# Kernel optimization log

Hardware: AMD Instinct MI355X
Metric: run time of the kernel (lower is better)

Reference implementation:

```python
import jax, jax.numpy as jnp
import numpy as np
from jax import lax

D_MODEL = 512
D_INNER = 1024   # expand=2
D_STATE = 16
D_CONV = 4
DT_RANK = 32     # ceil(d_model/16)
D_FFN = 2048
EPS = 1e-6


def _layernorm(x, g, b):
    mu = jnp.mean(x, axis=-1, keepdims=True)
    var = jnp.mean((x - mu) ** 2, axis=-1, keepdims=True)
    return (x - mu) * lax.rsqrt(var + EPS) * g + b


def _mamba(x, in_w, conv_w, conv_b, xproj_w, dt_w, dt_b, A_log, D_vec, out_w):
    # x: [B, L, d_model]
    B, L, _ = x.shape
    xz = jnp.einsum('bld,ed->ble', x, in_w)           # [B, L, 2*d_inner]
    xc, z = xz[..., :D_INNER], xz[..., D_INNER:]
    # causal depthwise conv over time
    xt = xc.transpose(0, 2, 1)                        # [B, d_inner, L]
    kern = conv_w[:, None, :]                         # [d_inner, 1, d_conv]
    xt = lax.conv_general_dilated(xt, kern, (1,), [(D_CONV - 1, 0)],
                                  feature_group_count=D_INNER)
    xc = jax.nn.silu(xt.transpose(0, 2, 1) + conv_b)  # [B, L, d_inner]
    # input-dependent SSM parameters
    x_dbl = jnp.einsum('bld,ed->ble', xc, xproj_w)    # [B, L, dt_rank+2*d_state]
    dt = x_dbl[..., :DT_RANK]
    Bm = x_dbl[..., DT_RANK:DT_RANK + D_STATE]
    Cm = x_dbl[..., DT_RANK + D_STATE:]
    delta = jax.nn.softplus(jnp.einsum('blr,dr->bld', dt, dt_w) + dt_b)  # [B, L, d_inner]
    A = -jnp.exp(A_log)                               # [d_inner, d_state]

    def step(h, inp):
        d_t, u_t, b_t, c_t = inp                      # [B,di],[B,di],[B,ds],[B,ds]
        dA = jnp.exp(d_t[:, :, None] * A)             # [B, di, ds]
        dBu = (d_t * u_t)[:, :, None] * b_t[:, None, :]
        h = dA * h + dBu
        y = jnp.einsum('bds,bs->bd', h, c_t)
        return h, y

    h0 = jnp.zeros((B, D_INNER, D_STATE), x.dtype)
    xs = (delta.transpose(1, 0, 2), xc.transpose(1, 0, 2),
          Bm.transpose(1, 0, 2), Cm.transpose(1, 0, 2))
    _, ys = lax.scan(step, h0, xs)                    # [L, B, d_inner]
    y = ys.transpose(1, 0, 2) + xc * D_vec
    y = y * jax.nn.silu(z)
    return jnp.einsum('ble,de->bld', y, out_w)        # [B, L, d_model]


def setup_inputs() -> dict:
    key = jax.random.key(0)
    ks = iter(jax.random.split(key, 40))
    B, S, T = 8, 512, 1024

    def nrm(shape, scale=0.02):
        return jax.random.normal(next(ks), shape, dtype=jnp.float32) * scale

    def mamba_params(prefix):
        A_log = jnp.log(jnp.broadcast_to(jnp.arange(1, D_STATE + 1, dtype=jnp.float32),
                                         (D_INNER, D_STATE)))
        return {
            prefix + '_in_w': nrm((2 * D_INNER, D_MODEL)),
            prefix + '_conv_w': nrm((D_INNER, D_CONV), 0.1),
            prefix + '_conv_b': jnp.zeros((D_INNER,), jnp.float32),
            prefix + '_xproj_w': nrm((DT_RANK + 2 * D_STATE, D_INNER)),
            prefix + '_dt_w': nrm((D_INNER, DT_RANK), 0.1),
            prefix + '_dt_b': jnp.full((D_INNER,), -4.0, jnp.float32),
            prefix + '_A_log': A_log,
            prefix + '_D_vec': jnp.ones((D_INNER,), jnp.float32),
            prefix + '_out_w': nrm((D_MODEL, D_INNER)),
        }

    inp = {
        'tgt': jax.random.normal(next(ks), (B, S, D_MODEL), dtype=jnp.float32),
        'memory': jax.random.normal(next(ks), (B, T, D_MODEL), dtype=jnp.float32),
    }
    inp.update(mamba_params('self'))
    inp.update(mamba_params('cross'))
    inp.update({
        'ln1_g': jnp.ones((D_MODEL,), jnp.float32), 'ln1_b': jnp.zeros((D_MODEL,), jnp.float32),
        'ln2_g': jnp.ones((D_MODEL,), jnp.float32), 'ln2_b': jnp.zeros((D_MODEL,), jnp.float32),
        'ln3_g': jnp.ones((D_MODEL,), jnp.float32), 'ln3_b': jnp.zeros((D_MODEL,), jnp.float32),
        'ffn_w1': nrm((D_FFN, D_MODEL)), 'ffn_b1': jnp.zeros((D_FFN,), jnp.float32),
        'ffn_w2': nrm((D_MODEL, D_FFN)), 'ffn_b2': jnp.zeros((D_MODEL,), jnp.float32),
    })
    return inp


def reference(tgt, memory,
              self_in_w, self_conv_w, self_conv_b, self_xproj_w, self_dt_w, self_dt_b,
              self_A_log, self_D_vec, self_out_w,
              cross_in_w, cross_conv_w, cross_conv_b, cross_xproj_w, cross_dt_w, cross_dt_b,
              cross_A_log, cross_D_vec, cross_out_w,
              ln1_g, ln1_b, ln2_g, ln2_b, ln3_g, ln3_b,
              ffn_w1, ffn_b1, ffn_w2, ffn_b2):
    S = tgt.shape[1]
    # self-Mamba block (post-norm, dropout=0)
    t2 = _mamba(tgt, self_in_w, self_conv_w, self_conv_b, self_xproj_w,
                self_dt_w, self_dt_b, self_A_log, self_D_vec, self_out_w)
    t = _layernorm(tgt + t2, ln1_g, ln1_b)
    # cross-Mamba: scan over [memory; tgt], keep last S steps
    cat = jnp.concatenate([memory, t], axis=1)
    c2 = _mamba(cat, cross_in_w, cross_conv_w, cross_conv_b, cross_xproj_w,
                cross_dt_w, cross_dt_b, cross_A_log, cross_D_vec, cross_out_w)[:, -S:]
    t = _layernorm(t + c2, ln2_g, ln2_b)
    # positionwise FFN
    f = jnp.einsum('bld,fd->blf', t, ffn_w1) + ffn_b1
    f = jax.nn.relu(f)
    f = jnp.einsum('blf,df->bld', f, ffn_w2) + ffn_b2
    t = _layernorm(t + f, ln3_g, ln3_b)
    return t
```

## Files before the change

kernel.cpp:

```cpp
#include <hip/hip_runtime.h>
#include <math.h>

#define DM    512
#define DI    1024
#define DSN   16
#define DTR   32
#define DFFN  2048
#define BB    8
#define SS    512
#define TTM   1024
#define LCAT  1536
#define CONV_R 8

#define ACT_NONE     0
#define ACT_RELU     1
#define ACT_DELTA    3
#define ACT_XDBL     4

typedef __attribute__((ext_vector_type(8))) short short8;
typedef __attribute__((ext_vector_type(8))) unsigned short ushort8;
typedef __attribute__((ext_vector_type(4))) float f32x4;

#define L2E 1.4426950408889634f

__device__ __forceinline__ unsigned short f2b(float f) {
    unsigned int u = __float_as_uint(f);
    return (unsigned short)((u + 0x7FFFu + ((u >> 16) & 1u)) >> 16);
}
__device__ __forceinline__ float b2f(unsigned short h) {
    return __uint_as_float(((unsigned int)h) << 16);
}
__device__ __forceinline__ float fast_softplus(float v) {
    return (v > 20.f) ? v : __logf(1.f + __expf(v));
}
__device__ __forceinline__ float fexp2(float x) {
#if __has_builtin(__builtin_amdgcn_exp2f)
    return __builtin_amdgcn_exp2f(x);
#else
    float r; asm("v_exp_f32 %0, %1" : "=v"(r) : "v"(x)); return r;
#endif
}
__device__ __forceinline__ float frcp(float x) {
    return __builtin_amdgcn_rcpf(x);
}
__device__ __forceinline__ void gld16(const void* g, void* l) {
    __builtin_amdgcn_global_load_lds(
        (const __attribute__((address_space(1))) void*)g,
        (__attribute__((address_space(3))) void*)l, 16, 0, 0);
}

__device__ __forceinline__ int map_row(int m, int mb, int bs, int ro) {
    int q = m / mb;
    return q * bs + ro + (m - q * mb);
}

__global__ __launch_bounds__(256) void mgemm_kernel(
    const unsigned short* __restrict__ A, int mb, int bs, int ro,
    const unsigned short* __restrict__ W, const float* __restrict__ bias,
    float* __restrict__ Cf, unsigned short* __restrict__ Cb,
    float* __restrict__ C2, float* __restrict__ Cf2,
    int N, int K, int act,
    int omb, int obs, int oro, int ldc, int nofs, int pstr,
    int ysplit, int amb2, int abs2, int aro2, int wofs2,
    int omb2, int obs2, int oro2, int nofs2)
{
    __shared__ __align__(16) unsigned short As[128 * 64];
    __shared__ __align__(16) unsigned short Bs[128 * 64];
    int tid = threadIdx.x;
    int lane = tid & 63, wave = tid >> 6;
    int wy = wave >> 1, wx = wave & 1;
    int bx = blockIdx.x, by = blockIdx.y;
    int nx = gridDim.x, ny = gridDim.y;
    const unsigned short* Wp = W;
    if (ysplit) {
        if (by >= ysplit) {
            by -= ysplit; ny = gridDim.y - ysplit;
            mb = amb2; bs = abs2; ro = aro2; Wp += wofs2;
            omb = omb2; obs = obs2; oro = oro2; nofs = nofs2;
        } else ny = ysplit;
    }
    int f = by * nx + bx;
    int xcd = f & 7, j2 = f >> 3;
    int bandh = ny >> 3;
    int m0 = (xcd * bandh + j2 / nx) * 128;
    int n0 = (j2 % nx) * 128;
    int Kh = K / gridDim.z;
    int kbeg = blockIdx.z * Kh, kend = kbeg + Kh;
    float* Cfo = Cf;
    const float* biaso = bias;
    if (blockIdx.z) { Cfo = Cf2 + (size_t)(blockIdx.z - 1) * pstr; biaso = nullptr; }

    unsigned aoff[4], boff[4];
    unsigned short* la[4];
    unsigned short* lb[4];
    #pragma unroll
    for (int j = 0; j < 4; j++) {
        int c  = wave * 256 + j * 64 + lane;
        int r  = c >> 3;
        int q  = c & 7;
        int g  = q ^ (r & 7);
        int arow = map_row(m0 + r, mb, bs, ro);
        aoff[j] = (unsigned)(arow * K + g * 8);
        boff[j] = (unsigned)((n0 + r) * K + g * 8);
        la[j] = As + (size_t)(wave * 256 + j * 64) * 8;
        lb[j] = Bs + (size_t)(wave * 256 + j * 64) * 8;
    }
    int fm = lane & 15, fg = lane >> 4;
    int sw = fg ^ (fm & 3);
    int b2 = (fm >> 2) & 1;
    const unsigned short* arp = As + ((size_t)(wy * 64 + fm) * 8 + sw) * 8;
    const unsigned short* brp = Bs + ((size_t)(wx * 64 + fm) * 8 + sw) * 8;

    f32x4 acc[4][4];
    #pragma unroll
    for (int i = 0; i < 4; i++)
        #pragma unroll
        for (int j = 0; j < 4; j++) acc[i][j] = 0.f;

    for (int k0 = kbeg; k0 < kend; k0 += 64) {
        #pragma unroll
        for (int j = 0; j < 4; j++) {
            gld16(A  + aoff[j] + k0, la[j]);
            gld16(Wp + boff[j] + k0, lb[j]);
        }
        __syncthreads();
        #pragma unroll
        for (int h = 0; h < 2; h++) {
            int ho = ((h ^ b2) * 32);
            short8 af[4], bfr[4];
            #pragma unroll
            for (int t = 0; t < 4; t++) af[t]  = *(const short8*)(arp + ho + t * 1024);
            #pragma unroll
            for (int t = 0; t < 4; t++) bfr[t] = *(const short8*)(brp + ho + t * 1024);
            #pragma unroll
            for (int i = 0; i < 4; i++)
                #pragma unroll
                for (int j = 0; j < 4; j++)
                    acc[i][j] = __builtin_amdgcn_mfma_f32_16x16x32_bf16(af[i], bfr[j], acc[i][j], 0, 0, 0);
        }
        __syncthreads();
    }

    int en = lane & 15, em = (lane >> 4) * 4;
    if (act == ACT_XDBL) {
        size_t zb = (size_t)blockIdx.z * omb;
        #pragma unroll
        for (int j = 0; j < 4; j++) {
            int n = n0 + wx * 64 + j * 16 + en;
            if (n >= 64) continue;
            #pragma unroll
            for (int i = 0; i < 4; i++) {
                int mbase = m0 + wy * 64 + i * 16 + em;
                #pragma unroll
                for (int r = 0; r < 4; r++)
                    C2[(zb + mbase + r) * 64 + n] = acc[i][j][r];
            }
        }
        return;
    }
    if (act == ACT_DELTA) {
        #pragma unroll
        for (int j = 0; j < 4; j++) {
            int n = n0 + wx * 64 + j * 16 + en;
            float bv = bias[n];
            #pragma unroll
            for (int i = 0; i < 4; i++) {
                int mbase = m0 + wy * 64 + i * 16 + em;
                #pragma unroll
                for (int r = 0; r < 4; r++) {
                    float v = acc[i][j][r] + bv;
                    Cb[(size_t)(mbase + r) * 1024 + n] = f2b(fast_softplus(v));
                }
            }
        }
        return;
    }
    #pragma unroll
    for (int j = 0; j < 4; j++) {
        int n = n0 + wx * 64 + j * 16 + en;
        float bv = biaso ? biaso[n] : 0.f;
        #pragma unroll
        for (int i = 0; i < 4; i++) {
            int mbase = m0 + wy * 64 + i * 16 + em;
            #pragma unroll
            for (int r = 0; r < 4; r++) {
                float v = acc[i][j][r] + bv;
                if (act == ACT_RELU) v = v > 0.f ? v : 0.f;
                int orow = map_row(mbase + r, omb, obs, oro);
                size_t off = (size_t)orow * ldc + nofs + n;
                if (Cb) Cb[off] = f2b(v);
                else    Cfo[off] = v;
            }
        }
    }
}

__global__ __launch_bounds__(256) void xdbl_combine(
    const float* __restrict__ pxd, unsigned short* __restrict__ dtb,
    float* __restrict__ bcout, int M, int Z)
{
    int idx = blockIdx.x * 256 + threadIdx.x;
    int m = idx >> 4, n4 = idx & 15;
    int n = n4 * 4;
    float4 s = make_float4(0.f, 0.f, 0.f, 0.f);
    for (int z = 0; z < Z; z++) {
        float4 p = *(const float4*)(pxd + ((size_t)z * M + m) * 64 + n);
        s.x += p.x; s.y += p.y; s.z += p.z; s.w += p.w;
    }
    if (n < 32) {
        ((ushort4*)(dtb + (size_t)m * 64))[n4] =
            make_ushort4(f2b(s.x), f2b(s.y), f2b(s.z), f2b(s.w));
    } else {
        *(float4*)(bcout + (size_t)m * 32 + (n - 32)) = s;
        ((ushort4*)(dtb + (size_t)m * 64))[n4] = make_ushort4(0, 0, 0, 0);
    }
}

struct PrepPtrs {
    const float* tgt; const float* mem;
    const float* w[6];
    const float* xpj_s; const float* xpj_c;
    const float* dtw_s; const float* dtw_c;
    unsigned short* tgtb; unsigned short* catb; unsigned short* wb;
    unsigned short* xprojb_s; unsigned short* xprojb_c;
    unsigned short* dtwb_s; unsigned short* dtwb_c;
};
__global__ __launch_bounds__(256) void prep_kernel(PrepPtrs p)
{
    int u = blockIdx.x * 256 + threadIdx.x;
    if (u < 524288) {
        float4 v = ((const float4*)p.tgt)[u];
        ((ushort4*)p.tgtb)[u] = make_ushort4(f2b(v.x), f2b(v.y), f2b(v.z), f2b(v.w));
        return;
    }
    if (u < 1572864) {
        int f = u - 524288;
        int b = f >> 17, rem = f & 131071;
        float4 v = ((const float4*)p.mem)[f];
        ((ushort4*)p.catb)[(size_t)b * 196608 + rem] =
            make_ushort4(f2b(v.x), f2b(v.y), f2b(v.z), f2b(v.w));
        return;
    }
    if (u < 2883584) {
        const int cum[7] = {0, 262144, 524288, 655360, 786432, 1048576, 1310720};
        int i = u - 1572864;
        int seg = 0;
        #pragma unroll
        for (int s = 1; s < 6; s++) seg += (i >= cum[s]);
        float4 v = ((const float4*)p.w[seg])[i - cum[seg]];
        ((ushort4*)p.wb)[i] = make_ushort4(f2b(v.x), f2b(v.y), f2b(v.z), f2b(v.w));
        return;
    }
    if (u < 2949120) {
        int i = u - 2883584;
        const float* src = p.xpj_s;
        unsigned short* dst = p.xprojb_s;
        if (i >= 32768) { i -= 32768; src = p.xpj_c; dst = p.xprojb_c; }
        int n = i >> 8;
        ushort4 o = make_ushort4(0, 0, 0, 0);
        if (n < 64) {
            float4 v = ((const float4*)src)[i];
            o = make_ushort4(f2b(v.x), f2b(v.y), f2b(v.z), f2b(v.w));
        }
        ((ushort4*)dst)[i] = o;
        return;
    }
    {
        int i = u - 2949120;
        const float* src = p.dtw_s;
        unsigned short* dst = p.dtwb_s;
        if (i >= 16384) { i -= 16384; src = p.dtw_c; dst = p.dtwb_c; }
        int n = i >> 4, c = (i & 15) * 4;
        ushort4 o = make_ushort4(0, 0, 0, 0);
        if (c < 32) {
            float4 v = *(const float4*)(src + n * 32 + c);
            o = make_ushort4(f2b(v.x), f2b(v.y), f2b(v.z), f2b(v.w));
        }
        ((ushort4*)dst)[i] = o;
    }
}

__global__ __launch_bounds__(256) void conv_silu_kernel(
    const unsigned short* __restrict__ xz,
    const float* __restrict__ cw,
    const float* __restrict__ cb,
    unsigned short* __restrict__ xc, int L, int total)
{
    int idx = blockIdx.x * blockDim.x + threadIdx.x;
    if (idx >= total) return;
    int d8 = idx & 127;
    int d0 = d8 * 8;
    int t  = idx >> 7;
    int nq = L / CONV_R;
    int b  = t / nq;
    int l0 = (t - b * nq) * CONV_R;
    size_t rbase = (size_t)b * L + l0;

    float4 wv[8];
    #pragma unroll
    for (int j = 0; j < 8; j++) wv[j] = *(const float4*)(cw + (d0 + j) * 4);
    float bias[8];
    {
        float4 c0 = ((const float4*)(cb + d0))[0];
        float4 c1 = ((const float4*)(cb + d0))[1];
        bias[0]=c0.x; bias[1]=c0.y; bias[2]=c0.z; bias[3]=c0.w;
        bias[4]=c1.x; bias[5]=c1.y; bias[6]=c1.z; bias[7]=c1.w;
    }
    ushort8 win[CONV_R + 3];
    #pragma unroll
    for (int k = 0; k < 3; k++) {
        ushort8 z;
        #pragma unroll
        for (int j = 0; j < 8; j++) z[j] = 0;
        win[k] = (l0 - 3 + k >= 0)
            ? *(const ushort8*)(xz + (rbase - 3 + k) * 2048 + d0) : z;
    }
    #pragma unroll
    for (int i = 0; i < CONV_R; i++)
        win[3 + i] = *(const ushort8*)(xz + (rbase + i) * 2048 + d0);

    const float* w = (const float*)&wv[0];
    #pragma unroll
    for (int i = 0; i < CONV_R; i++) {
        float acc[8];
        #pragma unroll
        for (int j = 0; j < 8; j++) acc[j] = bias[j];
        #pragma unroll
        for (int k = 0; k < 4; k++) {
            ushort8 v = win[i + k];
            #pragma unroll
            for (int j = 0; j < 8; j++)
                acc[j] = fmaf(b2f(v[j]), w[j * 4 + k], acc[j]);
        }
        ushort8 o;
        #pragma unroll
        for (int j = 0; j < 8; j++)
            o[j] = f2b(acc[j] * frcp(1.f + __expf(-acc[j])));
        *(ushort8*)(xc + (rbase + i) * 1024 + d0) = o;
    }
}

__global__ __launch_bounds__(256) void scan_part1(
    const unsigned short* __restrict__ delta, const unsigned short* __restrict__ xc,
    const float* __restrict__ bc, const float* __restrict__ A_log,
    float* __restrict__ part_h, float* __restrict__ part_s, int L, int CH, int NCr)
{
    int tid = threadIdx.x;
    int dblk = blockIdx.x & 3;
    int rest = blockIdx.x >> 2;
    int c    = rest % NCr;
    int b    = rest / NCr;
    if (c == NCr - 1) return;
    int d    = dblk * 256 + tid;
    float A2[DSN];
    {
        const float4* ap = (const float4*)(A_log + d * DSN);
        #pragma unroll
        for (int q = 0; q < 4; q++) {
            float4 a4 = ap[q];
            A2[q*4+0] = -__expf(a4.x) * L2E;
            A2[q*4+1] = -__expf(a4.y) * L2E;
            A2[q*4+2] = -__expf(a4.z) * L2E;
            A2[q*4+3] = -__expf(a4.w) * L2E;
        }
    }
    float h[DSN];
    #pragma unroll
    for (int s = 0; s < DSN; s++) h[s] = 0.f;
    float ssum = 0.f;
    int l0 = c * CH;
    for (int l = l0; l < l0 + CH; l++) {
        size_t r = (size_t)b * L + l;
        float4 bq[4];
        const float4* bp = (const float4*)(bc + r * 32);
        #pragma unroll
        for (int q = 0; q < 4; q++) bq[q] = bp[q];
        const float* Bm = (const float*)&bq[0];
        float dl = b2f(delta[r * DI + d]);
        float u  = b2f(xc[r * DI + d]);
        float du = dl * u;
        ssum += dl;
        #pragma unroll
        for (int s = 0; s < DSN; s++)
            h[s] = fmaf(fexp2(dl * A2[s]), h[s], du * Bm[s]);
    }
    size_t base = ((size_t)(b * NCr + c) * DI + d) * DSN;
    #pragma unroll
    for (int q = 0; q < 4; q++)
        ((float4*)(part_h + base))[q] = make_float4(h[q*4], h[q*4+1], h[q*4+2], h[q*4+3]);
    part_s[(size_t)(b * NCr + c) * DI + d] = ssum;
}

__global__ __launch_bounds__(256) void scan_combine(
    const float* __restrict__ A_log,
    float* __restrict__ part_h, const float* __restrict__ part_s, int NCr)
{
    int idx = blockIdx.x * 256 + threadIdx.x;
    int s  = idx & (DSN - 1);
    int dd = (idx >> 4) & (DI - 1);
    int b  = idx >> 14;
    float A2 = -__expf(A_log[dd * DSN + s]) * L2E;
    float h = 0.f;
    size_t sbase = (size_t)b * NCr * DI + dd;
    size_t hbase = ((size_t)b * NCr * DI + dd) * DSN + s;
    for (int c = 0; c < NCr; c++) {
        float ph = part_h[hbase];
        float S  = part_s[sbase];
        part_h[hbase] = h;
        h = fmaf(fexp2(A2 * S), h, ph);
        hbase += (size_t)DI * DSN;
        sbase += DI;
    }
}

__global__ __launch_bounds__(256) void scan_part2(
    const unsigned short* __restrict__ delta, const unsigned short* __restrict__ xc,
    const float* __restrict__ bc, const unsigned short* __restrict__ xz,
    const float* __restrict__ A_log, const float* __restrict__ Dv,
    const float* __restrict__ part_h,
    unsigned short* __restrict__ out, int L, int CH, int NCr, int c0, int lmin)
{
    int tid = threadIdx.x;
    int dblk = blockIdx.x & 3;
    int rest = blockIdx.x >> 2;
    int ncp  = NCr - c0;
    int c    = c0 + rest % ncp;
    int b    = rest / ncp;
    int d    = dblk * 256 + tid;
    float A2[DSN];
    {
        const float4* ap = (const float4*)(A_log + d * DSN);
        #pragma unroll
        for (int q = 0; q < 4; q++) {
            float4 a4 = ap[q];
            A2[q*4+0] = -__expf(a4.x) * L2E;
            A2[q*4+1] = -__expf(a4.y) * L2E;
            A2[q*4+2] = -__expf(a4.z) * L2E;
            A2[q*4+3] = -__expf(a4.w) * L2E;
        }
    }
    float Dvd = Dv[d];
    size_t base = ((size_t)(b * NCr + c) * DI + d) * DSN;
    float h4[4][4];
    #pragma unroll
    for (int q = 0; q < 4; q++) *((float4*)h4[q]) = ((const float4*)(part_h + base))[q];
    float h[DSN];
    #pragma unroll
    for (int s = 0; s < DSN; s++) h[s] = h4[s >> 2][s & 3];
    int l0 = c * CH;
    for (int l = l0; l < l0 + CH; l++) {
        size_t r = (size_t)b * L + l;
        float4 bq[8];
        const float4* bp = (const float4*)(bc + r * 32);
        #pragma unroll
        for (int q = 0; q < 8; q++) bq[q] = bp[q];
        const float* Bm = (const float*)&bq[0];
        const float* Cm = Bm + DSN;
        float dl = b2f(delta[r * DI + d]);
        float u  = b2f(xc[r * DI + d]);
        float du = dl * u;
        float y = 0.f;
        #pragma unroll
        for (int s = 0; s < DSN; s++) {
            h[s] = fmaf(fexp2(dl * A2[s]), h[s], du * Bm[s]);
            y = fmaf(h[s], Cm[s], y);
        }
        if (l >= lmin) {
            float z = b2f(xz[r * 2048 + DI + d]);
            float sil = z * frcp(1.f + __expf(-z));
            out[r * DI + d] = f2b((y + u * Dvd) * sil);
        }
    }
}

__global__ __launch_bounds__(128) void addln_kernel(
    const float* __restrict__ a, int amb, int absd, int aro, int lda,
    const float* __restrict__ bsrc, const float* __restrict__ parts, int nparts, int pstr,
    const float* __restrict__ g, const float* __restrict__ be,
    float* __restrict__ outf, int omb, int obsd, int oro, int ldo,
    unsigned short* __restrict__ outb, int bmb, int bbsd, int bro, int ldb)
{
    int m = blockIdx.x, t = threadIdx.x;
    int ar = map_row(m, amb, absd, aro);
    float4 x4 = ((const float4*)(a + (size_t)ar * lda))[t];
    float4 y4 = ((const float4*)(bsrc + (size_t)m * DM))[t];
    float v[4] = {x4.x + y4.x, x4.y + y4.y, x4.z + y4.z, x4.w + y4.w};
    for (int p = 0; p < nparts; p++) {
        float4 z4 = ((const float4*)(parts + (size_t)p * pstr + (size_t)m * DM))[t];
        v[0] += z4.x; v[1] += z4.y; v[2] += z4.z; v[3] += z4.w;
    }
    float sum = v[0] + v[1] + v[2] + v[3];
    float sq  = v[0]*v[0] + v[1]*v[1] + v[2]*v[2] + v[3]*v[3];
    #pragma unroll
    for (int o = 32; o > 0; o >>= 1) {
        sum += __shfl_down(sum, o);
        sq  += __shfl_down(sq, o);
    }
    __shared__ float s0[2], s1[2];
    if ((t & 63) == 0) { s0[t >> 6] = sum; s1[t >> 6] = sq; }
    __syncthreads();
    float tot = s0[0] + s0[1];
    float tsq = s1[0] + s1[1];
    float mu = tot * (1.f / DM);
    float var = tsq * (1.f / DM) - mu * mu;
    float rs = rsqrtf(var + 1e-6f);
    float4 g4 = ((const float4*)g)[t];
    float4 b4 = ((const float4*)be)[t];
    float o0 = (v[0] - mu) * rs * g4.x + b4.x;
    float o1 = (v[1] - mu) * rs * g4.y + b4.y;
    float o2 = (v[2] - mu) * rs * g4.z + b4.z;
    float o3 = (v[3] - mu) * rs * g4.w + b4.w;
    if (outf) {
        int orow = map_row(m, omb, obsd, oro);
        ((float4*)(outf + (size_t)orow * ldo))[t] = make_float4(o0, o1, o2, o3);
    }
    if (outb) {
        int brow = map_row(m, bmb, bbsd, bro);
        ((ushort4*)(outb + (size_t)brow * ldb))[t] =
            make_ushort4(f2b(o0), f2b(o1), f2b(o2), f2b(o3));
    }
}

static void run_scan(const unsigned short* dltb, const unsigned short* xcb, const float* bc,
                     const unsigned short* xzb, const float* A_log, const float* Dv,
                     float* part_h, float* part_s, unsigned short* out, int L, int NCr,
                     int c0, int lmin, hipStream_t stream)
{
    int CH = L / NCr;
    int blocks1 = BB * NCr * (DI / 256);
    scan_part1<<<blocks1, 256, 0, stream>>>(dltb, xcb, bc, A_log, part_h, part_s, L, CH, NCr);
    scan_combine<<<BB * DI * DSN / 256, 256, 0, stream>>>(A_log, part_h, part_s, NCr);
    int blocks2 = BB * (NCr - c0) * (DI / 256);
    scan_part2<<<blocks2, 256, 0, stream>>>(dltb, xcb, bc, xzb, A_log, Dv, part_h, out, L, CH, NCr, c0, lmin);
}

extern "C" void kernel_launch(void* const* d_in, const int* in_sizes, int n_in,
                              void* d_out, int out_size, void* d_ws, size_t ws_size,
                              hipStream_t stream)
{
    const float* tgt       = (const float*)d_in[0];
    const float* memory    = (const float*)d_in[1];
    const float* s_in_w    = (const float*)d_in[2];
    const float* s_conv_w  = (const float*)d_in[3];
    const float* s_conv_b  = (const float*)d_in[4];
    const float* s_xproj_w = (const float*)d_in[5];
    const float* s_dt_w    = (const float*)d_in[6];
    const float* s_dt_b    = (const float*)d_in[7];
    const float* s_A_log   = (const float*)d_in[8];
    const float* s_D_vec   = (const float*)d_in[9];
    const float* s_out_w   = (const float*)d_in[10];
    const float* c_in_w    = (const float*)d_in[11];
    const float* c_conv_w  = (const float*)d_in[12];
    const float* c_conv_b  = (const float*)d_in[13];
    const float* c_xproj_w = (const float*)d_in[14];
    const float* c_dt_w    = (const float*)d_in[15];
    const float* c_dt_b    = (const float*)d_in[16];
    const float* c_A_log   = (const float*)d_in[17];
    const float* c_D_vec   = (const float*)d_in[18];
    const float* c_out_w   = (const float*)d_in[19];
    const float* ln1_g     = (const float*)d_in[20];
    const float* ln1_b     = (const float*)d_in[21];
    const float* ln2_g     = (const float*)d_in[22];
    const float* ln2_b     = (const float*)d_in[23];
    const float* ln3_g     = (const float*)d_in[24];
    const float* ln3_b     = (const float*)d_in[25];
    const float* ffn_w1    = (const float*)d_in[26];
    const float* ffn_b1    = (const float*)d_in[27];
    const float* ffn_w2    = (const float*)d_in[28];
    const float* ffn_b2    = (const float*)d_in[29];
    float* outp = (float*)d_out;

    float* ws     = (float*)d_ws;
    float* bc     = ws;
    float* t1     = bc     + 393216;
    float* tbuf   = t1     + 2097152;
    float* part_h = tbuf   + 2097152;
    float* proj   = part_h;
    float* pparts = part_h + 2097152;
    float* pxd    = part_h;
    float* part_s = part_h + 8388608;
    unsigned short* ub      = (unsigned short*)(part_s + 524288);
    unsigned short* dltb    = ub;
    unsigned short* catb    = dltb    + 12582912;
    unsigned short* tgtb    = catb    + 6291456;
    unsigned short* xzb     = tgtb    + 2097152;
    unsigned short* xcb     = xzb     + 25165824;
    unsigned short* ygb     = xcb     + 12582912;
    unsigned short* tbbf    = ygb     + 12582912;
    unsigned short* s_in_wb = tbbf    + 2097152;
    unsigned short* c_in_wb = s_in_wb + 1048576;
    unsigned short* s_out_wb= c_in_wb + 1048576;
    unsigned short* c_out_wb= s_out_wb+ 524288;
    unsigned short* w1b     = c_out_wb+ 524288;
    unsigned short* w2b     = w1b     + 1048576;
    unsigned short* xprojb_s= w2b     + 1048576;
    unsigned short* xprojb_c= xprojb_s+ 131072;
    unsigned short* dtwb_s  = xprojb_c+ 131072;
    unsigned short* dtwb_c  = dtwb_s  + 65536;
    unsigned short* dtb     = dtwb_c  + 65536;
    unsigned short* fbuf    = xzb;
    float* ffnout  = (float*)dltb;
    float* fparts  = ffnout + 2097152;

    {
        PrepPtrs pp;
        pp.tgt = tgt; pp.mem = memory;
        pp.w[0]=s_in_w; pp.w[1]=c_in_w; pp.w[2]=s_out_w; pp.w[3]=c_out_w; pp.w[4]=ffn_w1; pp.w[5]=ffn_w2;
        pp.xpj_s = s_xproj_w; pp.xpj_c = c_xproj_w;
        pp.dtw_s = s_dt_w;    pp.dtw_c = c_dt_w;
        pp.tgtb = tgtb; pp.catb = catb; pp.wb = s_in_wb;
        pp.xprojb_s = xprojb_s; pp.xprojb_c = xprojb_c;
        pp.dtwb_s = dtwb_s; pp.dtwb_c = dtwb_c;
        prep_kernel<<<11648, 256, 0, stream>>>(pp);
    }

    mgemm_kernel<<<dim3(2048/128, 4096/128), 256, 0, stream>>>(
        tgtb, 4096, 0, 0, s_in_wb, nullptr, nullptr, xzb, nullptr, nullptr, 2048, 512, ACT_NONE,
        4096, 0, 0, 2048, 0, 0,  0, 0,0,0, 0, 0,0,0, 0);
    conv_silu_kernel<<<(BB*(SS/CONV_R)*128 + 255)/256, 256, 0, stream>>>(
        xzb, s_conv_w, s_conv_b, xcb, SS, BB*(SS/CONV_R)*128);
    mgemm_kernel<<<dim3(1, 4096/128, 4), 256, 0, stream>>>(
        xcb, 4096, 0, 0, xprojb_s, nullptr, nullptr, nullptr, pxd, nullptr, 128, 1024, ACT_XDBL,
        4096, 0, 0, 0, 0, 0,  0, 0,0,0, 0, 0,0,0, 0);
    xdbl_combine<<<4096*16/256, 256, 0, stream>>>(pxd, dtb, bc, 4096, 4);
    mgemm_kernel<<<dim3(1024/128, 4096/128), 256, 0, stream>>>(
        dtb, 4096, 0, 0, dtwb_s, s_dt_b, nullptr, dltb, nullptr, nullptr, 1024, 64, ACT_DELTA,
        4096, 0, 0, 1024, 0, 0,  0, 0,0,0, 0, 0,0,0, 0);
    run_scan(dltb, xcb, bc, xzb, s_A_log, s_D_vec, part_h, part_s, ygb, SS, 32, 0, 0, stream);
    mgemm_kernel<<<dim3(512/128, 4096/128, 4), 256, 0, stream>>>(
        ygb, 4096, 0, 0, s_out_wb, nullptr, proj, nullptr, nullptr, pparts, 512, 1024, ACT_NONE,
        4096, 0, 0, 512, 0, 2097152,  0, 0,0,0, 0, 0,0,0, 0);
    addln_kernel<<<4096, 128, 0, stream>>>(
        tgt, 4096, 0, 0, DM, proj, pparts, 3, 2097152, ln1_g, ln1_b,
        t1, 4096, 0, 0, DM, catb, 512, 1536, 1024, DM);

    mgemm_kernel<<<dim3(1024/128, 96 + 32), 256, 0, stream>>>(
        catb, 12288, 0, 0, c_in_wb, nullptr, nullptr, xzb, nullptr, nullptr, 2048, 512, ACT_NONE,
        12288, 0, 0, 2048, 0, 0,
        96, 512, 1536, 1024, 1024 * 512, 512, 1536, 1024, 1024);
    conv_silu_kernel<<<(BB*(LCAT/CONV_R)*128 + 255)/256, 256, 0, stream>>>(
        xzb, c_conv_w, c_conv_b, xcb, LCAT, BB*(LCAT/CONV_R)*128);
    mgemm_kernel<<<dim3(1, 12288/128, 4), 256, 0, stream>>>(
        xcb, 12288, 0, 0, xprojb_c, nullptr, nullptr, nullptr, pxd, nullptr, 128, 1024, ACT_XDBL,
        12288, 0, 0, 0, 0, 0,  0, 0,0,0, 0, 0,0,0, 0);
    xdbl_combine<<<12288*16/256, 256, 0, stream>>>(pxd, dtb, bc, 12288, 4);
    mgemm_kernel<<<dim3(1024/128, 12288/128), 256, 0, stream>>>(
        dtb, 12288, 0, 0, dtwb_c, c_dt_b, nullptr, dltb, nullptr, nullptr, 1024, 64, ACT_DELTA,
        12288, 0, 0, 1024, 0, 0,  0, 0,0,0, 0, 0,0,0, 0);
    run_scan(dltb, xcb, bc, xzb, c_A_log, c_D_vec, part_h, part_s, ygb, LCAT, 32, 21, 1024, stream);
    mgemm_kernel<<<dim3(512/128, 4096/128, 4), 256, 0, stream>>>(
        ygb, 512, 1536, 1024, c_out_wb, nullptr, proj, nullptr, nullptr, pparts, 512, 1024, ACT_NONE,
        4096, 0, 0, 512, 0, 2097152,  0, 0,0,0, 0, 0,0,0, 0);
    addln_kernel<<<4096, 128, 0, stream>>>(
        t1, 4096, 0, 0, DM, proj, pparts, 3, 2097152, ln2_g, ln2_b,
        tbuf, 4096, 0, 0, DM, tbbf, 4096, 0, 0, DM);

    mgemm_kernel<<<dim3(2048/128, 4096/128), 256, 0, stream>>>(
        tbbf, 4096, 0, 0, w1b, ffn_b1, nullptr, fbuf, nullptr, nullptr, 2048, 512, ACT_RELU,
        4096, 0, 0, 2048, 0, 0,  0, 0,0,0, 0, 0,0,0, 0);
    mgemm_kernel<<<dim3(512/128, 4096/128, 4), 256, 0, stream>>>(
        fbuf, 4096, 0, 0, w2b, ffn_b2, ffnout, nullptr, nullptr, fparts, 512, 2048, ACT_NONE,
        4096, 0, 0, 512, 0, 2097152,  0, 0,0,0, 0, 0,0,0, 0);
    addln_kernel<<<4096, 128, 0, stream>>>(
        tbuf, 4096, 0, 0, DM, ffnout, fparts, 3, 2097152, ln3_g, ln3_b,
        outp, 4096, 0, 0, DM, nullptr, 0, 0, 0, 0);
}
```

Measured before the change: 498.9 us.

## Stage scan B/C in shared memory, prefetch inputs, and double chunk count

```diff
diff --git a/kernel.cpp b/kernel.cpp
--- a/kernel.cpp
+++ b/kernel.cpp
@@ -345,12 +345,19 @@
     const float* __restrict__ bc, const float* __restrict__ A_log,
     float* __restrict__ part_h, float* __restrict__ part_s, int L, int CH, int NCr)
 {
+    __shared__ float bcs[24 * 16];
     int tid = threadIdx.x;
     int dblk = blockIdx.x & 3;
     int rest = blockIdx.x >> 2;
     int c    = rest % NCr;
     int b    = rest / NCr;
     if (c == NCr - 1) return;
+    int l0 = c * CH;
+    for (int i = tid; i < CH * 16; i += 256) {
+        int lr = i >> 4, s = i & 15;
+        bcs[i] = bc[((size_t)b * L + l0 + lr) * 32 + s];
+    }
+    __syncthreads();
     int d    = dblk * 256 + tid;
     float A2[DSN];
     {
@@ -368,21 +375,22 @@
     #pragma unroll
     for (int s = 0; s < DSN; s++) h[s] = 0.f;
     float ssum = 0.f;
-    int l0 = c * CH;
-    for (int l = l0; l < l0 + CH; l++) {
-        size_t r = (size_t)b * L + l;
-        float4 bq[4];
-        const float4* bp = (const float4*)(bc + r * 32);
-        #pragma unroll
-        for (int q = 0; q < 4; q++) bq[q] = bp[q];
-        const float* Bm = (const float*)&bq[0];
-        float dl = b2f(delta[r * DI + d]);
-        float u  = b2f(xc[r * DI + d]);
-        float du = dl * u;
-        ssum += dl;
+    size_t rb = (size_t)b * L + l0;
+    float dl = b2f(delta[rb * DI + d]);
+    float u  = b2f(xc[rb * DI + d]);
+    for (int i = 0; i < CH; i++) {
+        float cdl = dl, cu = u;
+        if (i + 1 < CH) {
+            size_t rn = rb + i + 1;
+            dl = b2f(delta[rn * DI + d]);
+            u  = b2f(xc[rn * DI + d]);
+        }
+        const float* Bm = bcs + i * 16;
+        float du = cdl * cu;
+        ssum += cdl;
         #pragma unroll
         for (int s = 0; s < DSN; s++)
-            h[s] = fmaf(fexp2(dl * A2[s]), h[s], du * Bm[s]);
+            h[s] = fmaf(fexp2(cdl * A2[s]), h[s], du * Bm[s]);
     }
     size_t base = ((size_t)(b * NCr + c) * DI + d) * DSN;
     #pragma unroll
@@ -420,12 +428,17 @@
     const float* __restrict__ part_h,
     unsigned short* __restrict__ out, int L, int CH, int NCr, int c0, int lmin)
 {
+    __shared__ float bcs[24 * 32];
     int tid = threadIdx.x;
     int dblk = blockIdx.x & 3;
     int rest = blockIdx.x >> 2;
     int ncp  = NCr - c0;
     int c    = c0 + rest % ncp;
     int b    = rest / ncp;
+    int l0 = c * CH;
+    for (int i = tid; i < CH * 32; i += 256)
+        bcs[i] = bc[((size_t)b * L + l0) * 32 + i];
+    __syncthreads();
     int d    = dblk * 256 + tid;
     float A2[DSN];
     {
@@ -447,28 +460,30 @@
     float h[DSN];
     #pragma unroll
     for (int s = 0; s < DSN; s++) h[s] = h4[s >> 2][s & 3];
-    int l0 = c * CH;
-    for (int l = l0; l < l0 + CH; l++) {
-        size_t r = (size_t)b * L + l;
-        float4 bq[8];
-        const float4* bp = (const float4*)(bc + r * 32);
-        #pragma unroll
-        for (int q = 0; q < 8; q++) bq[q] = bp[q];
-        const float* Bm = (const float*)&bq[0];
+    size_t rb = (size_t)b * L + l0;
+    float dl = b2f(delta[rb * DI + d]);
+    float u  = b2f(xc[rb * DI + d]);
+    float z  = b2f(xz[rb * 2048 + DI + d]);
+    for (int i = 0; i < CH; i++) {
+        float cdl = dl, cu = u, cz = z;
+        if (i + 1 < CH) {
+            size_t rn = rb + i + 1;
+            dl = b2f(delta[rn * DI + d]);
+            u  = b2f(xc[rn * DI + d]);
+            z  = b2f(xz[rn * 2048 + DI + d]);
+        }
+        const float* Bm = bcs + i * 32;
         const float* Cm = Bm + DSN;
-        float dl = b2f(delta[r * DI + d]);
-        float u  = b2f(xc[r * DI + d]);
-        float du = dl * u;
+        float du = cdl * cu;
         float y = 0.f;
         #pragma unroll
         for (int s = 0; s < DSN; s++) {
-            h[s] = fmaf(fexp2(dl * A2[s]), h[s], du * Bm[s]);
+            h[s] = fmaf(fexp2(cdl * A2[s]), h[s], du * Bm[s]);
             y = fmaf(h[s], Cm[s], y);
         }
-        if (l >= lmin) {
-            float z = b2f(xz[r * 2048 + DI + d]);
-            float sil = z * frcp(1.f + __expf(-z));
-            out[r * DI + d] = f2b((y + u * Dvd) * sil);
+        if (l0 + i >= lmin) {
+            float sil = cz * frcp(1.f + __expf(-cz));
+            out[(rb + i) * DI + d] = f2b((y + cu * Dvd) * sil);
         }
     }
 }
@@ -626,7 +641,7 @@
     mgemm_kernel<<<dim3(1024/128, 4096/128), 256, 0, stream>>>(
         dtb, 4096, 0, 0, dtwb_s, s_dt_b, nullptr, dltb, nullptr, nullptr, 1024, 64, ACT_DELTA,
         4096, 0, 0, 1024, 0, 0,  0, 0,0,0, 0, 0,0,0, 0);
-    run_scan(dltb, xcb, bc, xzb, s_A_log, s_D_vec, part_h, part_s, ygb, SS, 32, 0, 0, stream);
+    run_scan(dltb, xcb, bc, xzb, s_A_log, s_D_vec, part_h, part_s, ygb, SS, 64, 0, 0, stream);
     mgemm_kernel<<<dim3(512/128, 4096/128, 4), 256, 0, stream>>>(
         ygb, 4096, 0, 0, s_out_wb, nullptr, proj, nullptr, nullptr, pparts, 512, 1024, ACT_NONE,
         4096, 0, 0, 512, 0, 2097152,  0, 0,0,0, 0, 0,0,0, 0);
@@ -647,7 +662,7 @@
     mgemm_kernel<<<dim3(1024/128, 12288/128), 256, 0, stream>>>(
         dtb, 12288, 0, 0, dtwb_c, c_dt_b, nullptr, dltb, nullptr, nullptr, 1024, 64, ACT_DELTA,
         12288, 0, 0, 1024, 0, 0,  0, 0,0,0, 0, 0,0,0, 0);
-    run_scan(dltb, xcb, bc, xzb, c_A_log, c_D_vec, part_h, part_s, ygb, LCAT, 32, 21, 1024, stream);
+    run_scan(dltb, xcb, bc, xzb, c_A_log, c_D_vec, part_h, part_s, ygb, LCAT, 64, 42, 1024, stream);
     mgemm_kernel<<<dim3(512/128, 4096/128, 4), 256, 0, stream>>>(
         ygb, 512, 1536, 1024, c_out_wb, nullptr, proj, nullptr, nullptr, pparts, 512, 1024, ACT_NONE,
         4096, 0, 0, 512, 0, 2097152,  0, 0,0,0, 0, 0,0,0, 0);
```

Result: no change. 495.9 us (-0.6%).
